# Optimization experiments

Measured on AMD Instinct MI355X. Metric: run time of the kernel, lower is better.

The kernel has to match this reference:

```python
import jax, jax.numpy as jnp
import numpy as np

N = 100000      # nodes
E = 1000000     # edges (before self loops)
F_IN = 128      # num_features
G = 512         # graphs in batch
NC = 10         # num_classes
EPS_BN = 1e-5
NEG_SLOPE = 0.2


def setup_inputs() -> dict:
    key = jax.random.key(0)
    ks = iter(jax.random.split(key, 40))
    rn = lambda shape, s=0.1: jax.random.normal(next(ks), shape, jnp.float32) * s
    inp = {
        "x": jax.random.normal(next(ks), (N, F_IN), jnp.float32),
        "edge_index": jax.random.randint(next(ks), (2, E), 0, N),
        "batch": jnp.sort(jax.random.randint(next(ks), (N,), 0, G)),
        "W1": rn((F_IN, 128)), "as1": rn((8, 16)), "ad1": rn((8, 16)), "b1": jnp.zeros((128,), jnp.float32),
        "g1": jnp.ones((128,), jnp.float32), "be1": jnp.zeros((128,), jnp.float32),
        "Wl1": rn((128, 16)), "bl1": jnp.zeros((16,), jnp.float32),
        "gl1": jnp.ones((16,), jnp.float32), "bel1": jnp.zeros((16,), jnp.float32),
        "W2": rn((16, 96)), "as2": rn((4, 24)), "ad2": rn((4, 24)), "b2": jnp.zeros((96,), jnp.float32),
        "g2": jnp.ones((96,), jnp.float32), "be2": jnp.zeros((96,), jnp.float32),
        "Wl2": rn((96, 24)), "bl2": jnp.zeros((24,), jnp.float32),
        "gl2": jnp.ones((24,), jnp.float32), "bel2": jnp.zeros((24,), jnp.float32),
        "W3": rn((24, 64)), "as3": rn((2, 32)), "ad3": rn((2, 32)), "b3": jnp.zeros((64,), jnp.float32),
        "g3": jnp.ones((64,), jnp.float32), "be3": jnp.zeros((64,), jnp.float32),
        # final classifier
        "Wo": rn((64, NC)), "bo": jnp.zeros((NC,), jnp.float32),
    }
    return inp


def _bn(h, gamma, beta):
    # training-mode BatchNorm1d: batch statistics, biased variance
    m = jnp.mean(h, axis=0)
    v = jnp.var(h, axis=0)
    return gamma * (h - m) * jax.lax.rsqrt(v + EPS_BN) + beta


def _gat(h_in, src, dst, W, a_src, a_dst, bias, n):
    heads, ch = a_src.shape
    h = (h_in @ W).reshape(n, heads, ch)                     # [N,H,C]
    alpha_s = jnp.sum(h * a_src, axis=-1)                    # [N,H]
    alpha_d = jnp.sum(h * a_dst, axis=-1)                    # [N,H]
    e = jax.nn.leaky_relu(alpha_s[src] + alpha_d[dst], NEG_SLOPE)   # [E,H]
    emax = jax.ops.segment_max(e, dst, num_segments=n)       # segment softmax over target
    e = jnp.exp(e - emax[dst])
    denom = jax.ops.segment_sum(e, dst, num_segments=n)
    alpha = e / (denom[dst] + 1e-16)                         # [E,H]
    msg = h[src] * alpha[:, :, None]                         # [E,H,C]
    out = jax.ops.segment_sum(msg, dst, num_segments=n)      # [N,H,C]
    return out.reshape(n, heads * ch) + bias


def reference(x, edge_index, batch,
              W1, as1, ad1, b1, g1, be1, Wl1, bl1, gl1, bel1,
              W2, as2, ad2, b2, g2, be2, Wl2, bl2, gl2, bel2,
              W3, as3, ad3, b3, g3, be3, Wo, bo):
    n = x.shape[0]
    loop = jnp.arange(n)
    src = jnp.concatenate([edge_index[0], loop])   # add self loops (PyG default)
    dst = jnp.concatenate([edge_index[1], loop])

    h = jax.nn.relu(_bn(_gat(x, src, dst, W1, as1, ad1, b1, n), g1, be1))
    h = jax.nn.relu(_bn(h @ Wl1 + bl1, gl1, bel1))
    h = jax.nn.relu(_bn(_gat(h, src, dst, W2, as2, ad2, b2, n), g2, be2))
    h = jax.nn.relu(_bn(h @ Wl2 + bl2, gl2, bel2))
    h = jax.nn.relu(_bn(_gat(h, src, dst, W3, as3, ad3, b3, n), g3, be3))

    # global mean pool over graphs
    counts = jax.ops.segment_sum(jnp.ones((n,), h.dtype), batch, num_segments=G)
    pooled = jax.ops.segment_sum(h, batch, num_segments=G) / jnp.maximum(counts, 1.0)[:, None]
    # dropout is identity in eval
    return pooled @ Wo + bo
```

## Files before the change

### kernel.cpp

```cpp
#include <hip/hip_runtime.h>

typedef unsigned short u16;
typedef unsigned int   u32;
typedef unsigned long long u64;
typedef __attribute__((ext_vector_type(8))) short short8;
typedef __attribute__((ext_vector_type(4))) float f32x4;

#define DEVI __device__ __forceinline__

#define NPB 256
#define SHB 8
#define BHB 64
#define PST 256
#define LOG2E 1.44269504088896340736f

DEVI float bf2f(u16 u){ union{u32 i; float f;} x; x.i = ((u32)u)<<16; return x.f; }
DEVI u16 f2bf(float f){ union{float f; u32 i;} x; x.f = f;
  u32 r = (x.i + 0x7FFFu + ((x.i>>16)&1u))>>16; return (u16)r; }
DEVI float lrelu(float x){ return x > 0.f ? x : 0.2f*x; }
DEVI float exp2g(float x){ return __builtin_amdgcn_exp2f(x); }
DEVI float gload(const void* p, size_t i, int f32){
  return f32 ? ((const float*)p)[i] : bf2f(((const u16*)p)[i]);
}

__global__ __launch_bounds__(256) void k_prep(const void* x, const void* W1,
    const void* W2, const void* as2, const void* ad2,
    const void* W3, const void* as3, const void* ad3,
    int* dflag, u16* Wt, u16* Wbd2, u16* Wbd3, float* prepF, int* cnts)
{
  __shared__ int sf32;
  if (threadIdx.x == 0){
    const u16* p = (const u16*)x;
    int hits = 0;
    for (int j = 0; j < 512; j++){
      u16 e = (p[j] >> 7) & 0xFF;
      if (e >= 0xC0) hits++;
    }
    sf32 = hits ? 1 : 0;
    if (blockIdx.x == 0) *dflag = sf32;
  }
  __syncthreads();
  const int f32 = sf32;
  int b = blockIdx.x, t = threadIdx.x;
  if (b < 16){
    for (int i = b*256 + t; i < 128*128; i += 16*256){
      int k = i >> 7, nn = i & 127;
      Wt[nn*128 + k] = f2bf(gload(W1, i, f32));
    }
  } else if (b == 16){
    for (int i = t; i < 64*96; i += 256){
      int r = i/96, m = i - r*96;
      int h = r >> 4, k = r & 15;
      float v = ((m/24) == h) ? gload(W2, k*96 + m, f32) : 0.f;
      Wbd2[i] = f2bf(v);
    }
    if (t < 64){
      int h = t >> 4, k = t & 15;
      float s = 0.f, d = 0.f;
      for (int c = 0; c < 24; c++){
        float w = gload(W2, k*96 + h*24 + c, f32);
        s = fmaf(w, gload(as2, h*24 + c, f32), s);
        d = fmaf(w, gload(ad2, h*24 + c, f32), d);
      }
      prepF[t] = s; prepF[64 + t] = d;
    }
  } else {
    for (int i = t; i < 48*64; i += 256){
      int r = i >> 6, m = i & 63;
      int h = r/24, k = r - h*24;
      float v = ((m >> 5) == h) ? gload(W3, k*64 + m, f32) : 0.f;
      Wbd3[i] = f2bf(v);
    }
    if (t < 48){
      int h = t/24, k = t - h*24;
      float s = 0.f, d = 0.f;
      for (int c = 0; c < 32; c++){
        float w = gload(W3, k*64 + h*32 + c, f32);
        s = fmaf(w, gload(as3, h*32 + c, f32), s);
        d = fmaf(w, gload(ad3, h*32 + c, f32), d);
      }
      prepF[128 + t] = s; prepF[176 + t] = d;
    }
    if (t >= 64 && t < 72) cnts[t - 64] = 0;
  }
}

__global__ __launch_bounds__(1024) void k_bhist(const int* ei, int E, int* hist, int NB){
  __shared__ int lh[512];
  for (int b = threadIdx.x; b < NB; b += 1024) lh[b] = 0;
  __syncthreads();
  for (int e = blockIdx.x*1024 + threadIdx.x; e < E; e += BHB*1024)
    atomicAdd(&lh[((u32)ei[E + e]) >> SHB], 1);
  __syncthreads();
  for (int b = threadIdx.x; b < NB; b += 1024) hist[blockIdx.x*NB + b] = lh[b];
}

__global__ __launch_bounds__(256) void k_btotW(const int* hist, int* tot, int NB){
  int wv = threadIdx.x >> 6, lane = threadIdx.x & 63;
  int b = blockIdx.x*4 + wv;
  if (b >= NB) return;
  int v = hist[lane*NB + b];
  #pragma unroll
  for (int st = 1; st < 64; st <<= 1) v += __shfl_xor(v, st);
  if (lane == 0) tot[b] = v;
}

__global__ __launch_bounds__(512) void k_bscan(const int* tot, int* base, int* coff, int NB, int N){
  __shared__ int l[512];
  int t = threadIdx.x;
  int v = (t < NB) ? tot[t] : 0;
  l[t] = v; __syncthreads();
  for (int st = 1; st < 512; st <<= 1){
    int a = (t >= st) ? l[t - st] : 0;
    __syncthreads();
    l[t] += a;
    __syncthreads();
  }
  if (t < NB) base[t] = l[t] - v;
  if (t == 511){ base[NB] = l[511]; coff[N] = l[511]; }
}

__global__ __launch_bounds__(256) void k_bcurW(int* hist, const int* base, int NB){
  int wv = threadIdx.x >> 6, lane = threadIdx.x & 63;
  int b = blockIdx.x*4 + wv;
  if (b >= NB) return;
  int v = hist[lane*NB + b];
  int sc = v;
  #pragma unroll
  for (int d = 1; d < 64; d <<= 1){
    int t2 = __shfl_up(sc, d);
    if (lane >= d) sc += t2;
  }
  hist[lane*NB + b] = base[b] + sc - v;
}

__global__ __launch_bounds__(1024) void k_bfill(const int* ei, int E, const int* hist,
                                                u32* tmp, int NB){
  __shared__ int cur[512];
  for (int b = threadIdx.x; b < NB; b += 1024) cur[b] = hist[blockIdx.x*NB + b];
  __syncthreads();
  for (int e = blockIdx.x*1024 + threadIdx.x; e < E; e += BHB*1024){
    int s = ei[e], d = ei[E + e];
    int p = atomicAdd(&cur[((u32)d) >> SHB], 1);
    tmp[p] = ((u32)(d & (NPB-1)) << 24) | (u32)s;
  }
}

__global__ __launch_bounds__(256) void k_cfill(const u32* tmp, const int* base,
                                               int* coff, int* csr, int N){
  __shared__ int cnt[NPB], start[NPB];
  int b = blockIdx.x, t = threadIdx.x;
  int p0 = base[b], p1 = base[b + 1];
  cnt[t] = 0;
  __syncthreads();
  for (int i = p0 + t; i < p1; i += 256)
    atomicAdd(&cnt[tmp[i] >> 24], 1);
  __syncthreads();
  if (t == 0){
    int run = p0;
    for (int j = 0; j < NPB; j++){ start[j] = run; run += cnt[j]; }
  }
  __syncthreads();
  {
    int node = b*NPB + t;
    if (node < N) coff[node] = start[t];
    cnt[t] = 0;
  }
  __syncthreads();
  for (int i = p0 + t; i < p1; i += 256){
    u32 pr = tmp[i];
    int dj = pr >> 24;
    int r = atomicAdd(&cnt[dj], 1);
    csr[start[dj] + r] = (int)(pr & 0xFFFFFFu);
  }
}

__global__ __launch_bounds__(256) void k_mfma1A(const void* x, const u16* __restrict__ Wt,
    const void* a_s, const void* a_d,
    u16* __restrict__ out, u16* __restrict__ als, u16* __restrict__ ald,
    int n, const int* dflag)
{
  const int f32 = dflag[0];
  const int wave = threadIdx.x >> 6;
  const int lane = threadIdx.x & 63;
  const int l15 = lane & 15, q = lane >> 4;
  const int arow = blockIdx.x*64 + wave*16 + l15;
  const bool rok = arow < n;

  f32x4 acc[8];
  #pragma unroll
  for (int t = 0; t < 8; t++) acc[t] = {0.f, 0.f, 0.f, 0.f};

  #pragma unroll
  for (int kk = 0; kk < 4; kk++){
    short8 a = {0,0,0,0,0,0,0,0};
    if (rok){
      const int ko = kk*32 + q*8;
      if (f32){
        const float* xp = (const float*)x + (size_t)arow*128 + ko;
        float4 v0 = *(const float4*)xp;
        float4 v1 = *(const float4*)(xp + 4);
        a[0]=(short)f2bf(v0.x); a[1]=(short)f2bf(v0.y); a[2]=(short)f2bf(v0.z); a[3]=(short)f2bf(v0.w);
        a[4]=(short)f2bf(v1.x); a[5]=(short)f2bf(v1.y); a[6]=(short)f2bf(v1.z); a[7]=(short)f2bf(v1.w);
      } else {
        a = *(const short8*)((const u16*)x + (size_t)arow*128 + ko);
      }
    }
    #pragma unroll
    for (int t = 0; t < 8; t++){
      short8 b = *(const short8*)(Wt + (size_t)(l15 + 16*t)*128 + kk*32 + q*8);
      acc[t] = __builtin_amdgcn_mfma_f32_16x16x32_bf16(a, b, acc[t], 0, 0, 0);
    }
  }

  const int orow0 = blockIdx.x*64 + wave*16 + q*4;
  #pragma unroll
  for (int r = 0; r < 4; r++){
    int orow = orow0 + r;
    if (orow < n){
      #pragma unroll
      for (int t = 0; t < 8; t++)
        out[(size_t)orow*128 + l15 + 16*t] = f2bf(acc[t][r]);
    }
  }

  float as_l[8], ad_l[8];
  #pragma unroll
  for (int t = 0; t < 8; t++){
    as_l[t] = gload(a_s, t*16 + l15, f32);
    ad_l[t] = gload(a_d, t*16 + l15, f32);
  }
  #pragma unroll
  for (int r = 0; r < 4; r++){
    float s[8], d[8];
    #pragma unroll
    for (int t = 0; t < 8; t++){
      s[t] = acc[t][r] * as_l[t];
      d[t] = acc[t][r] * ad_l[t];
    }
    #pragma unroll
    for (int st = 1; st < 16; st <<= 1){
      #pragma unroll
      for (int t = 0; t < 8; t++){
        s[t] += __shfl_xor(s[t], st);
        d[t] += __shfl_xor(d[t], st);
      }
    }
    int orow = orow0 + r;
    if (l15 == 0 && orow < n){
      short8 sv, dv;
      #pragma unroll
      for (int t = 0; t < 8; t++){
        sv[t] = (short)f2bf(s[t] * LOG2E);
        dv[t] = (short)f2bf(d[t] * LOG2E);
      }
      *(short8*)(als + (size_t)orow*8) = sv;
      *(short8*)(ald + (size_t)orow*8) = dv;
    }
  }
}

template<int K,int M,int RT,int TPB,bool AFFINE,bool WBF16>
__global__ __launch_bounds__(TPB) void k_gemm(
    const u16* in, const void* Wg,
    const float* stat, const void* gam, const void* bet, float invn,
    u16* out, int n, const int* dflag)
{
  constexpr int CT = 4;
  constexpr int TC = M/CT;
  constexpr int TR = TPB/TC;
  constexpr int ROWS = TR*RT;
  static_assert(TPB % TC == 0, "");
  __shared__ __align__(16) u16 Wl[K*M];
  __shared__ float Il[ROWS*(K+1)];
  __shared__ float faL[AFFINE ? K : 1], fdL[AFFINE ? K : 1];

  const int f32 = dflag[0];
  if constexpr (AFFINE){
    for (int k = threadIdx.x; k < K; k += TPB){
      float m = stat[k]*invn;
      float vv = stat[128 + k]*invn - m*m;
      float a = gload(gam, k, f32) * rsqrtf(vv + 1e-5f);
      faL[k] = a;
      fdL[k] = gload(bet, k, f32) - m*a;
    }
    __syncthreads();
  }

  for (int i = threadIdx.x; i < K*M; i += TPB){
    if constexpr (WBF16) Wl[i] = ((const u16*)Wg)[i];
    else Wl[i] = f32 ? f2bf(((const float*)Wg)[i]) : ((const u16*)Wg)[i];
  }

  const int rowbase = blockIdx.x * ROWS;
  for (int i = threadIdx.x; i < ROWS*K; i += TPB){
    int rr = i / K, k = i - rr*K;
    int r = rowbase + rr;
    float v = 0.f;
    if (r < n){
      v = bf2f(in[(size_t)r*K + k]);
      if constexpr (AFFINE) v = fmaxf(fmaf(faL[k], v, fdL[k]), 0.f);
    }
    Il[rr*(K+1) + k] = v;
  }
  __syncthreads();

  const int tc = threadIdx.x % TC;
  const int tr = threadIdx.x / TC;
  float acc[RT][CT];
  #pragma unroll
  for (int j = 0; j < RT; j++)
    #pragma unroll
    for (int c = 0; c < CT; c++) acc[j][c] = 0.f;

  #pragma unroll 8
  for (int k = 0; k < K; k++){
    ushort4 u = *(const ushort4*)&Wl[k*M + tc*CT];
    float w0 = bf2f(u.x), w1 = bf2f(u.y), w2 = bf2f(u.z), w3 = bf2f(u.w);
    #pragma unroll
    for (int j = 0; j < RT; j++){
      float iv = Il[(tr + j*TR)*(K+1) + k];
      acc[j][0] = fmaf(iv, w0, acc[j][0]);
      acc[j][1] = fmaf(iv, w1, acc[j][1]);
      acc[j][2] = fmaf(iv, w2, acc[j][2]);
      acc[j][3] = fmaf(iv, w3, acc[j][3]);
    }
  }

  #pragma unroll
  for (int j = 0; j < RT; j++){
    int r = rowbase + tr + j*TR;
    if (r < n){
      ushort4 st;
      st.x = f2bf(acc[j][0]); st.y = f2bf(acc[j][1]);
      st.z = f2bf(acc[j][2]); st.w = f2bf(acc[j][3]);
      *(ushort4*)&out[(size_t)r*M + tc*CT] = st;
    }
  }
}

template<int H,int C>
__global__ __launch_bounds__(256) void k_pullW(const u16* __restrict__ h,
    const u16* __restrict__ als, const u16* __restrict__ ald,
    const int* __restrict__ off, const int* __restrict__ csr, u16* __restrict__ out, int n)
{
  constexpr int F = H*C;
  constexpr int L = F/2;
  constexpr int LOGH = (H==8)?3:((H==4)?2:1);
  constexpr int EPG = 64 >> LOGH;
  int wid = blockIdx.x*4 + (threadIdx.x >> 6);
  if (wid >= n) return;
  int lane = threadIdx.x & 63;
  int uu = lane >> LOGH;
  int hh = lane & (H-1);
  int fl = (lane < L) ? lane : (L-1);
  int hd = (2*fl)/C;
  const u32* hw = (const u32*)h;

  float adw = bf2f(ald[(u32)wid*H + hh]);
  float wsw = exp2g(lrelu(bf2f(als[(u32)wid*H + hh]) + adw));
  float den_lane = (uu == 0) ? wsw : 0.f;

  float wsf = exp2g(lrelu(bf2f(als[(u32)wid*H + hd]) + bf2f(ald[(u32)wid*H + hd])));
  u32 vs = hw[(u32)wid*L + fl];
  float acc0 = wsf * bf2f((u16)vs);
  float acc1 = wsf * bf2f((u16)(vs >> 16));

  int e0 = off[wid], e1 = off[wid + 1];
  for (int e = e0; e < e1; e += EPG){
    int rem = e1 - e;
    int su = csr[e + (uu < rem ? uu : 0)];
    float w = exp2g(lrelu(bf2f(als[(u32)su*H + hh]) + adw));
    if (uu >= rem) w = 0.f;
    den_lane += w;
    int cnt = rem < EPG ? rem : EPG;
    for (int jj = 0; jj < cnt; jj += 8){
      int sb[8]; float wb[8]; u32 vv[8];
      #pragma unroll
      for (int j = 0; j < 8; j++){
        int sl = ((jj + j) << LOGH) + hd;
        sb[j] = __shfl(su, sl);
        wb[j] = __shfl(w,  sl);
      }
      #pragma unroll
      for (int j = 0; j < 8; j++) vv[j] = hw[(u32)sb[j]*L + fl];
      #pragma unroll
      for (int j = 0; j < 8; j++){
        acc0 = fmaf(wb[j], bf2f((u16)vv[j]), acc0);
        acc1 = fmaf(wb[j], bf2f((u16)(vv[j] >> 16)), acc1);
      }
    }
  }
  #pragma unroll
  for (int st = H; st < 64; st <<= 1) den_lane += __shfl_xor(den_lane, st);
  float den = __shfl(den_lane, hd);
  float r = 1.f/(den + 1e-16f);
  if (lane < L)
    ((u32*)out)[(u32)wid*L + fl] = (u32)f2bf(acc0*r) | ((u32)f2bf(acc1*r) << 16);
}

template<int H,int CIN>
__global__ __launch_bounds__(256) void k_alphaX(const u16* __restrict__ Cb,
    const float* stat, const void* gam, const void* bet, float invn,
    const float* vs, const float* vd,
    u16* act, u16* als, u16* ald, int n, const int* dflag)
{
  constexpr int L2 = CIN/2;
  const int f32 = dflag[0];
  __shared__ float faL[CIN], fdL[CIN];
  if (threadIdx.x < CIN){
    int k = threadIdx.x;
    float m = stat[k]*invn;
    float vv = stat[128 + k]*invn - m*m;
    float a = gload(gam, k, f32) * rsqrtf(vv + 1e-5f);
    faL[k] = a;
    fdL[k] = gload(bet, k, f32) - m*a;
  }
  __syncthreads();
  int idx = blockIdx.x*256 + threadIdx.x;
  if (idx >= n*H) return;
  int j = idx / H, h = idx - j*H;
  const u32* row32 = (const u32*)Cb + (size_t)j*L2;
  u32* act32 = (u32*)act + (size_t)j*L2;
  float s = 0.f, d = 0.f;
  #pragma unroll
  for (int k2 = 0; k2 < L2; k2++){
    u32 v = row32[k2];
    float v0 = fmaxf(fmaf(faL[2*k2],     bf2f((u16)v),         fdL[2*k2]),     0.f);
    float v1 = fmaxf(fmaf(faL[2*k2 + 1], bf2f((u16)(v >> 16)), fdL[2*k2 + 1]), 0.f);
    s = fmaf(v0, vs[h*CIN + 2*k2], s); s = fmaf(v1, vs[h*CIN + 2*k2 + 1], s);
    d = fmaf(v0, vd[h*CIN + 2*k2], d); d = fmaf(v1, vd[h*CIN + 2*k2 + 1], d);
    if (h == 0) act32[k2] = (u32)f2bf(v0) | ((u32)f2bf(v1) << 16);
  }
  als[idx] = f2bf(s * LOG2E); ald[idx] = f2bf(d * LOG2E);
}

template<int H,int CIN>
__global__ __launch_bounds__(256) void k_pullX(const u16* __restrict__ act,
    const u16* __restrict__ als, const u16* __restrict__ ald,
    const int* __restrict__ off, const int* __restrict__ csr, u16* __restrict__ D, int n)
{
  constexpr int LX = H*CIN;
  constexpr int LOGH = (H==4)?2:1;
  constexpr int EPG = 64 >> LOGH;
  int wid = blockIdx.x*4 + (threadIdx.x >> 6);
  if (wid >= n) return;
  int lane = threadIdx.x & 63;
  int uu = lane >> LOGH;
  int hh = lane & (H-1);
  int fl = (lane < LX) ? lane : (LX-1);
  int hf = fl / CIN, k = fl - hf*CIN;

  float adw = bf2f(ald[(u32)wid*H + hh]);
  float wsw = exp2g(lrelu(bf2f(als[(u32)wid*H + hh]) + adw));
  float den_lane = (uu == 0) ? wsw : 0.f;

  float wsf = exp2g(lrelu(bf2f(als[(u32)wid*H + hf]) + bf2f(ald[(u32)wid*H + hf])));
  float acc = wsf * bf2f(act[(u32)wid*CIN + k]);

  int e0 = off[wid], e1 = off[wid + 1];
  for (int e = e0; e < e1; e += EPG){
    int rem = e1 - e;
    int su = csr[e + (uu < rem ? uu : 0)];
    float w = exp2g(lrelu(bf2f(als[(u32)su*H + hh]) + adw));
    if (uu >= rem) w = 0.f;
    den_lane += w;
    int cnt = rem < EPG ? rem : EPG;
    for (int jj = 0; jj < cnt; jj += 8){
      int sb[8]; float wb[8]; u16 vv[8];
      #pragma unroll
      for (int j = 0; j < 8; j++){
        int sl = ((jj + j) << LOGH) + hf;
        sb[j] = __shfl(su, sl);
        wb[j] = __shfl(w,  sl);
      }
      #pragma unroll
      for (int j = 0; j < 8; j++) vv[j] = act[(u32)sb[j]*CIN + k];
      #pragma unroll
      for (int j = 0; j < 8; j++) acc = fmaf(wb[j], bf2f(vv[j]), acc);
    }
  }
  #pragma unroll
  for (int st = H; st < 64; st <<= 1) den_lane += __shfl_xor(den_lane, st);
  float den = __shfl(den_lane, hf);
  if (lane < LX)
    D[(u32)wid*LX + fl] = f2bf(acc / (den + 1e-16f));
}

template<int F,int TPB>
__global__ __launch_bounds__(TPB) void k_statAB(const u16* __restrict__ x, int n,
    float* __restrict__ part, float* __restrict__ outS, int* __restrict__ cnt)
{
  constexpr int L = F/2;
  constexpr int RPB = TPB/L;
  static_assert(TPB % L == 0, "");
  int c = threadIdx.x % L;
  int tr = threadIdx.x / L;
  const u32* xw = (const u32*)x;
  int chunk = (n + (int)gridDim.x - 1)/(int)gridDim.x;
  int r0 = blockIdx.x*chunk;
  int r1 = r0 + chunk; if (r1 > n) r1 = n;
  float a0=0.f, a1=0.f, b0=0.f, b1=0.f;
  int r = r0 + tr;
  for (; r + 3*RPB < r1; r += 4*RPB){
    u32 v0 = xw[(size_t)r*L + c];
    u32 v1 = xw[(size_t)(r + RPB)*L + c];
    u32 v2 = xw[(size_t)(r + 2*RPB)*L + c];
    u32 v3 = xw[(size_t)(r + 3*RPB)*L + c];
    float f0 = bf2f((u16)v0), f1 = bf2f((u16)(v0 >> 16));
    float f2 = bf2f((u16)v1), f3 = bf2f((u16)(v1 >> 16));
    float f4 = bf2f((u16)v2), f5 = bf2f((u16)(v2 >> 16));
    float f6 = bf2f((u16)v3), f7 = bf2f((u16)(v3 >> 16));
    a0 += (f0 + f2) + (f4 + f6);
    a1 += (f1 + f3) + (f5 + f7);
    b0 += (f0*f0 + f2*f2) + (f4*f4 + f6*f6);
    b1 += (f1*f1 + f3*f3) + (f5*f5 + f7*f7);
  }
  for (; r < r1; r += RPB){
    u32 v = xw[(size_t)r*L + c];
    float f0 = bf2f((u16)v), f1 = bf2f((u16)(v >> 16));
    a0 += f0; b0 = fmaf(f0, f0, b0);
    a1 += f1; b1 = fmaf(f1, f1, b1);
  }
  __shared__ float l0[TPB], l1[TPB], l2[TPB], l3[TPB];
  l0[threadIdx.x] = a0; l1[threadIdx.x] = a1;
  l2[threadIdx.x] = b0; l3[threadIdx.x] = b1;
  __syncthreads();
  for (int t2 = threadIdx.x; t2 < 256; t2 += TPB){
    int col = t2 & 127;
    float s = 0.f;
    if (col < F){
      int cc = col >> 1, par = col & 1;
      const float* base = (t2 >= 128) ? (par ? l3 : l2) : (par ? l1 : l0);
      #pragma unroll 4
      for (int j = 0; j < RPB; j++) s += base[j*L + cc];
    }
    part[(size_t)blockIdx.x*256 + t2] = s;
  }
  __threadfence();
  __shared__ int lastf;
  if (threadIdx.x == 0) lastf = (atomicAdd(cnt, 1) == (int)gridDim.x - 1) ? 1 : 0;
  __syncthreads();
  if (lastf){
    __threadfence();
    for (int t2 = threadIdx.x; t2 < 256; t2 += TPB){
      float s = 0.f;
      int b = 0;
      for (; b + 3 < PST; b += 4)
        s += (part[(size_t)b*256 + t2] + part[(size_t)(b+1)*256 + t2])
           + (part[(size_t)(b+2)*256 + t2] + part[(size_t)(b+3)*256 + t2]);
      for (; b < PST; b++) s += part[(size_t)b*256 + t2];
      outS[t2] = s;
    }
  }
}

__global__ __launch_bounds__(256) void k_pool(const u16* B, const int* batch, int n,
    const float* stat, const void* g3, const void* be3, float invn,
    const void* Wo, const void* bo, void* outp, const int* dflag)
{
  const int f32 = dflag[0];
  __shared__ float fa[64], fd[64];
  if (threadIdx.x < 64){
    int k = threadIdx.x;
    float m = stat[k]*invn;
    float v = stat[128 + k]*invn - m*m;
    float a = gload(g3, k, f32) * rsqrtf(v + 1e-5f);
    fa[k] = a;
    fd[k] = gload(be3, k, f32) - m*a;
  }
  __syncthreads();

  int g = blockIdx.x;
  int lane = threadIdx.x & 63, wv = threadIdx.x >> 6;
  int s, e;
  { int l = 0, h = n; while (l < h){ int m = (l+h)>>1; if (batch[m] <  g) l = m+1; else h = m; } s = l; }
  { int l = s, h = n; while (l < h){ int m = (l+h)>>1; if (batch[m] <= g) l = m+1; else h = m; } e = l; }
  float a = fa[lane], d = fd[lane], acc = 0.f;
  for (int r = s + wv; r < e; r += 4)
    acc += fmaxf(fmaf(a, bf2f(B[(size_t)r*64 + lane]), d), 0.f);
  __shared__ float pl[4][64];
  pl[wv][lane] = acc;
  __syncthreads();
  if (wv == 0){
    float cnt = (e > s) ? (float)(e - s) : 1.f;
    pl[0][lane] = (pl[0][lane] + pl[1][lane] + pl[2][lane] + pl[3][lane]) / cnt;
  }
  __syncthreads();
  if (threadIdx.x < 10){
    int lo = threadIdx.x;
    float o = gload(bo, lo, f32);
    for (int l2 = 0; l2 < 64; l2++) o = fmaf(pl[0][l2], gload(Wo, l2*10 + lo, f32), o);
    if (f32) ((float*)outp)[g*10 + lo] = o;
    else     ((u16*) outp)[g*10 + lo] = f2bf(o);
  }
}

extern "C" void kernel_launch(void* const* d_in, const int* in_sizes, int n_in,
                              void* d_out, int out_size, void* d_ws, size_t ws_size,
                              hipStream_t stream)
{
  const void* x   = d_in[0];
  const int* ei   = (const int*)d_in[1];
  const int* batch= (const int*)d_in[2];
  const void* W1  = d_in[3];
  const void* as1 = d_in[4];
  const void* ad1 = d_in[5];
  const void* g1  = d_in[7];
  const void* be1 = d_in[8];
  const void* Wl1 = d_in[9];
  const void* gl1 = d_in[11];
  const void* bel1= d_in[12];
  const void* W2  = d_in[13];
  const void* as2 = d_in[14];
  const void* ad2 = d_in[15];
  const void* g2  = d_in[17];
  const void* be2 = d_in[18];
  const void* Wl2 = d_in[19];
  const void* gl2 = d_in[21];
  const void* bel2= d_in[22];
  const void* W3  = d_in[23];
  const void* as3 = d_in[24];
  const void* ad3 = d_in[25];
  const void* g3  = d_in[27];
  const void* be3 = d_in[28];
  const void* Wo  = d_in[29];
  const void* bo  = d_in[30];
  (void)n_in; (void)ws_size;

  const int N = in_sizes[2];
  const int E = in_sizes[1] / 2;
  const int G = out_size / 10;
  const int NB = (N + NPB - 1) >> SHB;

  char* w = (char*)d_ws;
  size_t off = 0;
  auto alloc = [&](size_t bytes)->void*{
    size_t o = off; off += (bytes + 255) & ~(size_t)255; return (void*)(w + o);
  };
  int*   dflag= (int*)alloc(4);
  int*   cnts = (int*)alloc(8*4);
  int*   coff = (int*)alloc((size_t)(N+1)*4);
  int*   csr  = (int*)alloc((size_t)E*4);
  int*   bbase= (int*)alloc((size_t)(NB+1)*4);
  int*   btot = (int*)alloc((size_t)NB*4);
  int*   hist = (int*)alloc((size_t)BHB*NB*4);
  float* stS  = (float*)alloc(1280*4);
  float* part = (float*)alloc((size_t)PST*256*4);
  float* prepF= (float*)alloc(256*4);
  u16*   Wt   = (u16*)alloc(128*128*2);
  u16*   Wbd2 = (u16*)alloc(64*96*2);
  u16*   Wbd3 = (u16*)alloc(48*64*2);
  u16*   als  = (u16*)alloc((size_t)N*8*2);
  u16*   ald  = (u16*)alloc((size_t)N*8*2);
  u16*   Cb   = (u16*)alloc((size_t)N*24*2);
  u16*   A    = (u16*)alloc((size_t)N*128*2);
  u16*   B    = (u16*)alloc((size_t)N*128*2);
  u32*   tmp  = (u32*)A;
  u16*   D    = A;
  u16*   act  = A + (size_t)N*64;

  const float invN = 1.f/(float)N;
  const int nbw = (NB + 3)/4;

  k_prep<<<18, 256, 0, stream>>>(x, W1, W2, as2, ad2, W3, as3, ad3,
                                 dflag, Wt, Wbd2, Wbd3, prepF, cnts);

  k_bhist<<<BHB, 1024, 0, stream>>>(ei, E, hist, NB);
  k_btotW<<<nbw, 256, 0, stream>>>(hist, btot, NB);
  k_bscan<<<1, 512, 0, stream>>>(btot, bbase, coff, NB, N);
  k_bcurW<<<nbw, 256, 0, stream>>>(hist, bbase, NB);
  k_bfill<<<BHB, 1024, 0, stream>>>(ei, E, hist, tmp, NB);
  k_cfill<<<NB, 256, 0, stream>>>(tmp, bbase, coff, csr, N);

  k_mfma1A<<<(N+63)/64, 256, 0, stream>>>(x, Wt, as1, ad1, A, als, ald, N, dflag);
  k_pullW<8,16><<<(N+3)/4, 256, 0, stream>>>(A, als, ald, coff, csr, B, N);
  k_statAB<128,256><<<PST, 256, 0, stream>>>(B, N, part, stS + 0, cnts + 0);

  k_gemm<128,16,1,256,true,false><<<(N+63)/64, 256, 0, stream>>>(
      B, Wl1, stS + 0, g1, be1, invN, Cb, N, dflag);
  k_statAB<16,256><<<PST, 256, 0, stream>>>(Cb, N, part, stS + 256, cnts + 1);

  k_alphaX<4,16><<<(N*4+255)/256, 256, 0, stream>>>(
      Cb, stS + 256, gl1, bel1, invN, prepF + 0, prepF + 64, act, als, ald, N, dflag);
  k_pullX<4,16><<<(N+3)/4, 256, 0, stream>>>(act, als, ald, coff, csr, D, N);
  k_gemm<64,96,2,192,false,true><<<(N+15)/16, 192, 0, stream>>>(
      D, Wbd2, nullptr, nullptr, nullptr, invN, B, N, dflag);
  k_statAB<96,192><<<PST, 192, 0, stream>>>(B, N, part, stS + 512, cnts + 2);

  k_gemm<96,24,2,192,true,false><<<(N+63)/64, 192, 0, stream>>>(
      B, Wl2, stS + 512, g2, be2, invN, Cb, N, dflag);
  k_statAB<24,192><<<PST, 192, 0, stream>>>(Cb, N, part, stS + 768, cnts + 3);

  k_alphaX<2,24><<<(N*2+255)/256, 256, 0, stream>>>(
      Cb, stS + 768, gl2, bel2, invN, prepF + 128, prepF + 176, act, als, ald, N, dflag);
  k_pullX<2,24><<<(N+3)/4, 256, 0, stream>>>(act, als, ald, coff, csr, D, N);
  k_gemm<48,64,2,256,false,true><<<(N+31)/32, 256, 0, stream>>>(
      D, Wbd3, nullptr, nullptr, nullptr, invN, B, N, dflag);
  k_statAB<64,256><<<PST, 256, 0, stream>>>(B, N, part, stS + 1024, cnts + 4);

  k_pool<<<G, 256, 0, stream>>>(B, batch, N, stS + 1024, g3, be3, invN, Wo, bo, d_out, dflag);
}
```

Baseline: 698.0 us.

## Prefetch next edge chunk in GAT aggregation, hoist A loads, pack bf16 stores

```diff
diff --git a/kernel.cpp b/kernel.cpp
--- a/kernel.cpp
+++ b/kernel.cpp
@@ -11,7 +11,7 @@
 #define NPB 256
 #define SHB 8
 #define BHB 64
-#define PST 256
+#define PST 512
 #define LOG2E 1.44269504088896340736f
 
 DEVI float bf2f(u16 u){ union{u32 i; float f;} x; x.i = ((u32)u)<<16; return x.f; }
@@ -187,29 +187,42 @@
   const int arow = blockIdx.x*64 + wave*16 + l15;
   const bool rok = arow < n;
 
+  short8 a4[4];
+  #pragma unroll
+  for (int kk = 0; kk < 4; kk++) a4[kk] = short8{0,0,0,0,0,0,0,0};
+  if (rok){
+    if (f32){
+      const float* xp = (const float*)x + (size_t)arow*128;
+      float4 xv[8];
+      #pragma unroll
+      for (int kk = 0; kk < 4; kk++){
+        xv[2*kk]   = *(const float4*)(xp + kk*32 + q*8);
+        xv[2*kk+1] = *(const float4*)(xp + kk*32 + q*8 + 4);
+      }
+      #pragma unroll
+      for (int kk = 0; kk < 4; kk++){
+        a4[kk][0]=(short)f2bf(xv[2*kk].x);   a4[kk][1]=(short)f2bf(xv[2*kk].y);
+        a4[kk][2]=(short)f2bf(xv[2*kk].z);   a4[kk][3]=(short)f2bf(xv[2*kk].w);
+        a4[kk][4]=(short)f2bf(xv[2*kk+1].x); a4[kk][5]=(short)f2bf(xv[2*kk+1].y);
+        a4[kk][6]=(short)f2bf(xv[2*kk+1].z); a4[kk][7]=(short)f2bf(xv[2*kk+1].w);
+      }
+    } else {
+      const u16* xp = (const u16*)x + (size_t)arow*128;
+      #pragma unroll
+      for (int kk = 0; kk < 4; kk++) a4[kk] = *(const short8*)(xp + kk*32 + q*8);
+    }
+  }
+
   f32x4 acc[8];
   #pragma unroll
   for (int t = 0; t < 8; t++) acc[t] = {0.f, 0.f, 0.f, 0.f};
 
   #pragma unroll
   for (int kk = 0; kk < 4; kk++){
-    short8 a = {0,0,0,0,0,0,0,0};
-    if (rok){
-      const int ko = kk*32 + q*8;
-      if (f32){
-        const float* xp = (const float*)x + (size_t)arow*128 + ko;
-        float4 v0 = *(const float4*)xp;
-        float4 v1 = *(const float4*)(xp + 4);
-        a[0]=(short)f2bf(v0.x); a[1]=(short)f2bf(v0.y); a[2]=(short)f2bf(v0.z); a[3]=(short)f2bf(v0.w);
-        a[4]=(short)f2bf(v1.x); a[5]=(short)f2bf(v1.y); a[6]=(short)f2bf(v1.z); a[7]=(short)f2bf(v1.w);
-      } else {
-        a = *(const short8*)((const u16*)x + (size_t)arow*128 + ko);
-      }
-    }
     #pragma unroll
     for (int t = 0; t < 8; t++){
       short8 b = *(const short8*)(Wt + (size_t)(l15 + 16*t)*128 + kk*32 + q*8);
-      acc[t] = __builtin_amdgcn_mfma_f32_16x16x32_bf16(a, b, acc[t], 0, 0, 0);
+      acc[t] = __builtin_amdgcn_mfma_f32_16x16x32_bf16(a4[kk], b, acc[t], 0, 0, 0);
     }
   }
 
@@ -217,10 +230,17 @@
   #pragma unroll
   for (int r = 0; r < 4; r++){
     int orow = orow0 + r;
-    if (orow < n){
-      #pragma unroll
-      for (int t = 0; t < 8; t++)
-        out[(size_t)orow*128 + l15 + 16*t] = f2bf(acc[t][r]);
+    u32 po[8];
+    #pragma unroll
+    for (int t = 0; t < 8; t++){
+      u32 bown = f2bf(acc[t][r]);
+      u32 both = __shfl_xor(bown, 1);
+      po[t] = bown | (both << 16);
+    }
+    if (orow < n && (l15 & 1) == 0){
+      u32* op = (u32*)(out + (size_t)orow*128);
+      #pragma unroll
+      for (int t = 0; t < 8; t++) op[(l15 >> 1) + 8*t] = po[t];
     }
   }
 
@@ -367,10 +387,22 @@
   float acc1 = wsf * bf2f((u16)(vs >> 16));
 
   int e0 = off[wid], e1 = off[wid + 1];
+  int su = 0; float bl = 0.f;
+  if (e0 < e1){
+    int rem = e1 - e0;
+    su = csr[e0 + (uu < rem ? uu : 0)];
+    bl = bf2f(als[(u32)su*H + hh]);
+  }
   for (int e = e0; e < e1; e += EPG){
     int rem = e1 - e;
-    int su = csr[e + (uu < rem ? uu : 0)];
-    float w = exp2g(lrelu(bf2f(als[(u32)su*H + hh]) + adw));
+    int cur = su; float blc = bl;
+    int en = e + EPG;
+    if (en < e1){
+      int remn = e1 - en;
+      su = csr[en + (uu < remn ? uu : 0)];
+      bl = bf2f(als[(u32)su*H + hh]);
+    }
+    float w = exp2g(lrelu(blc + adw));
     if (uu >= rem) w = 0.f;
     den_lane += w;
     int cnt = rem < EPG ? rem : EPG;
@@ -379,8 +411,8 @@
       #pragma unroll
       for (int j = 0; j < 8; j++){
         int sl = ((jj + j) << LOGH) + hd;
-        sb[j] = __shfl(su, sl);
-        wb[j] = __shfl(w,  sl);
+        sb[j] = __shfl(cur, sl);
+        wb[j] = __shfl(w,   sl);
       }
       #pragma unroll
       for (int j = 0; j < 8; j++) vv[j] = hw[(u32)sb[j]*L + fl];
@@ -459,10 +491,22 @@
   float acc = wsf * bf2f(act[(u32)wid*CIN + k]);
 
   int e0 = off[wid], e1 = off[wid + 1];
+  int su = 0; float bl = 0.f;
+  if (e0 < e1){
+    int rem = e1 - e0;
+    su = csr[e0 + (uu < rem ? uu : 0)];
+    bl = bf2f(als[(u32)su*H + hh]);
+  }
   for (int e = e0; e < e1; e += EPG){
     int rem = e1 - e;
-    int su = csr[e + (uu < rem ? uu : 0)];
-    float w = exp2g(lrelu(bf2f(als[(u32)su*H + hh]) + adw));
+    int cur = su; float blc = bl;
+    int en = e + EPG;
+    if (en < e1){
+      int remn = e1 - en;
+      su = csr[en + (uu < remn ? uu : 0)];
+      bl = bf2f(als[(u32)su*H + hh]);
+    }
+    float w = exp2g(lrelu(blc + adw));
     if (uu >= rem) w = 0.f;
     den_lane += w;
     int cnt = rem < EPG ? rem : EPG;
@@ -471,8 +515,8 @@
       #pragma unroll
       for (int j = 0; j < 8; j++){
         int sl = ((jj + j) << LOGH) + hf;
-        sb[j] = __shfl(su, sl);
-        wb[j] = __shfl(w,  sl);
+        sb[j] = __shfl(cur, sl);
+        wb[j] = __shfl(w,   sl);
       }
       #pragma unroll
       for (int j = 0; j < 8; j++) vv[j] = act[(u32)sb[j]*CIN + k];
```

After: 785.9 us. +12.6%, slower.
